# Kernel tuning notes

Measured on AMD Instinct MI355X. Metric: run time of the kernel, lower is better.

## Reference

```python
import jax, jax.numpy as jnp
import numpy as np

B, N = 16, 2048
NOTE, BEAT_H, MEAS_H, FINAL_H = 512, 128, 64, 128
NUM_BEATS, NUM_MEAS = 256, 64
OUT = 11            # output_size; QPM_INDEX = 0
QPM = 0


def _uniform(k, shape, fan):
    b = 1.0 / np.sqrt(fan)
    return jax.random.uniform(k, shape, jnp.float32, -b, b)


def _lstm_cell(x, h, c, wih, whh, bih, bhh):
    g = x @ wih.T + bih + h @ whh.T + bhh
    ii, ff, gg, oo = jnp.split(g, 4, axis=-1)
    c2 = jax.nn.sigmoid(ff) * c + jax.nn.sigmoid(ii) * jnp.tanh(gg)
    return jax.nn.sigmoid(oo) * jnp.tanh(c2), c2


def setup_inputs() -> dict:
    key = jax.random.key(0)
    ks = jax.random.split(key, 20)
    note_emb = jax.random.normal(ks[0], (B, N, NOTE), jnp.float32)
    beat_emb = jax.random.normal(ks[1], (B, NUM_BEATS, BEAT_H), jnp.float32)
    measure_emb = jax.random.normal(ks[2], (B, NUM_MEAS, MEAS_H), jnp.float32)
    beat_numbers = jnp.sort(jax.random.randint(ks[3], (B, N), 0, NUM_BEATS), axis=1)
    measure_numbers = beat_numbers // (NUM_BEATS // NUM_MEAS)
    tin = BEAT_H + MEAS_H + 1 + (OUT - 1)   # beat-tempo LSTM input size
    fin = NOTE + BEAT_H + MEAS_H + OUT      # final LSTM input size
    d = OUT - 1
    return {
        "note_emb": note_emb, "beat_emb": beat_emb, "measure_emb": measure_emb,
        "beat_numbers": beat_numbers, "measure_numbers": measure_numbers,
        "Wa": _uniform(ks[4], (d, d), d), "ba": _uniform(ks[5], (d,), d),
        "ctx": _uniform(ks[6], (d,), d),
        "Wih_t": _uniform(ks[7], (4 * BEAT_H, tin), BEAT_H),
        "Whh_t": _uniform(ks[8], (4 * BEAT_H, BEAT_H), BEAT_H),
        "bih_t": _uniform(ks[9], (4 * BEAT_H,), BEAT_H),
        "bhh_t": _uniform(ks[10], (4 * BEAT_H,), BEAT_H),
        "Wih_f": _uniform(ks[11], (4 * FINAL_H, fin), FINAL_H),
        "Whh_f": _uniform(ks[12], (4 * FINAL_H, FINAL_H), FINAL_H),
        "bih_f": _uniform(ks[13], (4 * FINAL_H,), FINAL_H),
        "bhh_f": _uniform(ks[14], (4 * FINAL_H,), FINAL_H),
        "W_fc": _uniform(ks[15], (d, FINAL_H), FINAL_H),
        "b_fc": _uniform(ks[16], (d,), FINAL_H),
        "W_tfc": _uniform(ks[17], (1, BEAT_H), BEAT_H),
        "b_tfc": _uniform(ks[18], (1,), BEAT_H),
    }


def _decode(note_emb, beat_emb, measure_emb, beat_numbers, measure_numbers,
            Wa, ba, ctx, Wih_t, Whh_t, bih_t, bhh_t,
            Wih_f, Whh_f, bih_f, bhh_f, W_fc, b_fc, W_tfc, b_tfc):
    Bn, Nn = note_emb.shape[0], note_emb.shape[1]
    d = W_fc.shape[0]  # OUT - 1
    zs_beat = jnp.maximum(beat_numbers - beat_numbers[:, :1], 0)
    zs_meas = jnp.maximum(measure_numbers - measure_numbers[:, :1], 0)
    diff = jnp.diff(beat_numbers, axis=1)
    # beat_changed: first step forced to 1, then diff of beat numbers
    changed_all = jnp.concatenate([jnp.ones((Bn, 1), diff.dtype), diff], axis=1) > 0
    pos = jnp.arange(Nn)
    bidx = jnp.arange(Bn)

    carry0 = (
        jnp.zeros((Bn, BEAT_H)), jnp.zeros((Bn, BEAT_H)),        # tempo h, c
        jnp.zeros((Bn, FINAL_H)), jnp.zeros((Bn, FINAL_H)),      # final h, c
        jnp.zeros((Bn, d + 1)),                                   # prev_out
        jnp.zeros((Bn, beat_emb.shape[1], d)),                    # beat_results
        jnp.zeros((Bn, Nn, d + 1)),                               # out_total
    )

    def step(carry, i):
        th, tc, fh, fc_, prev_out, beat_results, out_total = carry
        changed = changed_all[:, i]                                # [B] bool
        # --- get_beat_corresp_out: notes j < i in the beat just finished ---
        prev_beat = beat_numbers[:, jnp.maximum(i - 1, 0)]         # [B]
        note_mask = (beat_numbers == prev_beat[:, None]) & (pos[None, :] < i)
        x = out_total[:, :, QPM + 1:]                              # [B,N,d]
        sim = (x @ Wa.T + ba) @ ctx                                # [B,N]
        sim = jnp.where(note_mask, sim, -1e9)
        w = jax.nn.softmax(sim, axis=1)
        result_node = jnp.einsum('bn,bnd->bd', w, x)
        result_node = jnp.where(note_mask.any(axis=1)[:, None], result_node, 0.0)
        cb = zs_beat[:, i]
        cm = zs_meas[:, i]
        # scatter result_node into beat_results only for batches whose beat changed
        old = beat_results[bidx, cb]
        beat_results = beat_results.at[bidx, cb].set(
            jnp.where(changed[:, None], result_node, old))
        # --- beat tempo RNN step (only applied where changed) ---
        tempo_in = jnp.concatenate([
            beat_emb[bidx, cb], measure_emb[bidx, cm],
            prev_out[:, QPM:QPM + 1], beat_results[bidx, cb]], axis=-1)
        th2, tc2 = _lstm_cell(tempo_in, th, tc, Wih_t, Whh_t, bih_t, bhh_t)
        th = jnp.where(changed[:, None], th2, th)
        tc = jnp.where(changed[:, None], tc2, tc)
        tmp_tempo = th2 @ W_tfc.T + b_tfc                          # [B,1]
        prev_out = prev_out.at[:, QPM:QPM + 1].set(
            jnp.where(changed[:, None], tmp_tempo, prev_out[:, QPM:QPM + 1]))
        # --- final note-level LSTM step (all batches) ---
        fin_in = jnp.concatenate([
            note_emb[:, i], beat_emb[bidx, cb], measure_emb[bidx, cm], prev_out], axis=-1)
        fh, fc_ = _lstm_cell(fin_in, fh, fc_, Wih_f, Whh_f, bih_f, bhh_f)
        out = fh @ W_fc.T + b_fc                                   # [B,d]
        prev_out = jnp.concatenate([prev_out[:, :QPM + 1], out], axis=-1)
        out_total = out_total.at[:, i].set(prev_out)
        return (th, tc, fh, fc_, prev_out, beat_results, out_total), None

    carry, _ = jax.lax.scan(step, carry0, jnp.arange(Nn))
    out_total = carry[-1]
    # zero out padded notes (note embedding all-zero rows)
    pad = (note_emb.sum(-1) == 0)[:, :, None]
    return jnp.where(pad, 0.0, out_total)


def reference(note_emb, beat_emb, measure_emb, beat_numbers, measure_numbers,
              Wa, ba, ctx, Wih_t, Whh_t, bih_t, bhh_t,
              Wih_f, Whh_f, bih_f, bhh_f, W_fc, b_fc, W_tfc, b_tfc):
    return _decode(note_emb, beat_emb, measure_emb, beat_numbers, measure_numbers,
                   Wa, ba, ctx, Wih_t, Whh_t, bih_t, bhh_t,
                   Wih_f, Whh_f, bih_f, bhh_f, W_fc, b_fc, W_tfc, b_tfc)
```

## Files before the change

### kernel.cpp

```cpp
#include <hip/hip_runtime.h>
#include <cstdint>
#include <cstddef>

#define B_      16
#define N_      2048
#define NOTE_   512
#define BEAT_H_ 128
#define MEAS_H_ 64
#define NBEATS_ 256
#define NMEAS_  64
#define OUT_    11
#define D_      10
#define TSTRIDE 136

typedef float f32x4 __attribute__((ext_vector_type(4)));
typedef unsigned int u32x4 __attribute__((ext_vector_type(4)));
typedef _Float16 h2v __attribute__((ext_vector_type(2)));

__device__ __forceinline__ float fexp2_(float x) {
#if __has_builtin(__builtin_amdgcn_exp2f)
    return __builtin_amdgcn_exp2f(x);
#else
    return exp2f(x);
#endif
}
__device__ __forceinline__ float frcp_(float x) {
#if __has_builtin(__builtin_amdgcn_rcpf)
    return __builtin_amdgcn_rcpf(x);
#else
    return 1.0f / x;
#endif
}
__device__ __forceinline__ float sigm_(float x) {
    return frcp_(1.0f + fexp2_(-1.4426950408889634f * x));
}
__device__ __forceinline__ float tanh_(float x) {
    return 1.0f - 2.0f * frcp_(fexp2_(2.8853900817779268f * x) + 1.0f);
}

__device__ __forceinline__ float dot2f_(unsigned wu, unsigned hu, float c) {
    union { unsigned u; h2v h; } a, bb;
    a.u = wu; bb.u = hu;
#if __has_builtin(__builtin_amdgcn_fdot2)
    return __builtin_amdgcn_fdot2(a.h, bb.h, c, false);
#else
    return c + (float)a.h[0] * (float)bb.h[0] + (float)a.h[1] * (float)bb.h[1];
#endif
}

__device__ __align__(16) _Float16 g_whh_h16[512 * 128];
__device__ float g_bias_eff[512];
__device__ float g_wtail0[512];
__device__ __align__(16) _Float16 g_wht_h16[512 * TSTRIDE];

__global__ __launch_bounds__(256) void pad_k(const float* __restrict__ note,
                                             int* __restrict__ padf) {
    int wave = threadIdx.x >> 6, lane = threadIdx.x & 63;
    int r = blockIdx.x * 4 + wave;
    const float* row = note + ((size_t)r << 9);
    float s = 0.f;
#pragma unroll
    for (int u = 0; u < 8; ++u) s += row[lane + (u << 6)];
#pragma unroll
    for (int off = 32; off; off >>= 1) s += __shfl_xor(s, off, 64);
    if (lane == 0) padf[r] = (s == 0.0f) ? 1 : 0;
}

__global__ __launch_bounds__(128) void fold_whh(
    const float* __restrict__ Whh_f, const float* __restrict__ Wih_f,
    const float* __restrict__ W_fc, const float* __restrict__ b_fc) {
    int gr = blockIdx.x;
    int t = threadIdx.x;
    __shared__ float tail[OUT_];
    if (t < OUT_) tail[t] = Wih_f[(size_t)gr * 715 + 704 + t];
    __syncthreads();
    float m = Whh_f[(size_t)gr * 128 + t];
#pragma unroll
    for (int d = 0; d < D_; ++d) m += tail[1 + d] * W_fc[d * 128 + t];
    g_whh_h16[(size_t)gr * 128 + t] = (_Float16)m;
    if (t == 0) {
        float bb = 0.f;
#pragma unroll
        for (int d = 0; d < D_; ++d) bb += tail[1 + d] * b_fc[d];
        g_bias_eff[gr] = bb;
        g_wtail0[gr] = tail[0];
    }
}

__global__ __launch_bounds__(128) void fold_wht(const float* __restrict__ Whh_t) {
    int gr = blockIdx.x, t = threadIdx.x;
    g_wht_h16[(size_t)gr * TSTRIDE + t] = (_Float16)Whh_t[(size_t)gr * 128 + t];
    if (t < TSTRIDE - 128) g_wht_h16[(size_t)gr * TSTRIDE + 128 + t] = (_Float16)0.f;
}

__global__ __launch_bounds__(256) void tempo_pre_k(
    const float* __restrict__ beat, const float* __restrict__ meas,
    const int* __restrict__ bnum, const int* __restrict__ mnum,
    const float* __restrict__ Wih_t, const float* __restrict__ bih_t,
    const float* __restrict__ bhh_t, float* __restrict__ tpre) {
    __shared__ float sin_[16][192];
    int b = blockIdx.x, qt = blockIdx.y;
    int t = threadIdx.x;
    int bn0 = bnum[b << 11], mn0 = mnum[b << 11];
    for (int idx = t; idx < 16 * 192; idx += 256) {
        int qq = idx / 192, kk = idx - qq * 192;
        int q = qt * 16 + qq;
        float v;
        if (kk < 128) {
            v = beat[(size_t)(b * NBEATS_ + q) * 128 + kk];
        } else {
            int cm = ((q + bn0) >> 2) - mn0;
            if (cm > 63) cm = 63;
            if (cm < 0) cm = 0;
            v = meas[(size_t)(b * NMEAS_ + cm) * 64 + (kk - 128)];
        }
        sin_[qq][kk] = v;
    }
    __syncthreads();
    for (int half = 0; half < 2; ++half) {
        int j = t + half * 256;
        const float* wr = Wih_t + (size_t)j * 203;
        float bias = bih_t[j] + bhh_t[j];
        float acc[16] = {};
        for (int k = 0; k < 192; ++k) {
            float w = wr[k];
#pragma unroll
            for (int qq = 0; qq < 16; ++qq) acc[qq] += w * sin_[qq][k];
        }
        for (int qq = 0; qq < 16; ++qq)
            tpre[(size_t)(b * NBEATS_ + qt * 16 + qq) * 512 + j] = acc[qq] + bias;
    }
}

__global__ __launch_bounds__(256) void fin_pre_gemm(
    const float* __restrict__ note, const float* __restrict__ beat,
    const float* __restrict__ meas, const int* __restrict__ bnum,
    const int* __restrict__ mnum, const float* __restrict__ Wih_f,
    const float* __restrict__ bih_f, const float* __restrict__ bhh_f,
    float* __restrict__ finp) {
    __shared__ float As[16][64];
    __shared__ float Bs[16][64];
    int t = threadIdx.x;
    int r0 = blockIdx.x * 64;
    int j0 = blockIdx.y * 64;

    int am = t >> 2, alane = t & 3;
    int r = r0 + am;
    int b = r >> 11;
    int rb = b << 11;
    int cb = bnum[r] - bnum[rb];
    int cm = mnum[r] - mnum[rb];
    const float* arow_note = note + ((size_t)r << 9);
    const float* arow_beat = beat + ((size_t)(b * NBEATS_ + cb) << 7);
    const float* arow_meas = meas + ((size_t)(b * NMEAS_ + cm) << 6);

    int jj = t >> 2, blane = t & 3;
    const float* brow = Wih_f + (size_t)(j0 + jj) * 715;

    int tm0 = (t & 15) * 4, tn0 = (t >> 4) * 4;
    float acc[4][4] = {};

    for (int k0 = 0; k0 < 704; k0 += 16) {
        int ka = k0 + alane * 4;
        float4 av;
        if (ka < 512)      av = *(const float4*)(arow_note + ka);
        else if (ka < 640) av = *(const float4*)(arow_beat + (ka - 512));
        else               av = *(const float4*)(arow_meas + (ka - 640));
        int kb = k0 + blane * 4;
        float b0 = brow[kb], b1 = brow[kb + 1], b2 = brow[kb + 2], b3 = brow[kb + 3];
        __syncthreads();
        As[alane * 4 + 0][am] = av.x;
        As[alane * 4 + 1][am] = av.y;
        As[alane * 4 + 2][am] = av.z;
        As[alane * 4 + 3][am] = av.w;
        Bs[blane * 4 + 0][jj] = b0;
        Bs[blane * 4 + 1][jj] = b1;
        Bs[blane * 4 + 2][jj] = b2;
        Bs[blane * 4 + 3][jj] = b3;
        __syncthreads();
#pragma unroll
        for (int kk = 0; kk < 16; ++kk) {
            float4 a4 = *(const float4*)&As[kk][tm0];
            float4 b4 = *(const float4*)&Bs[kk][tn0];
            float aa[4] = {a4.x, a4.y, a4.z, a4.w};
            float bb[4] = {b4.x, b4.y, b4.z, b4.w};
#pragma unroll
            for (int mi = 0; mi < 4; ++mi)
#pragma unroll
                for (int ni = 0; ni < 4; ++ni) acc[mi][ni] += aa[mi] * bb[ni];
        }
    }
    float bias[4], beff[4];
#pragma unroll
    for (int ni = 0; ni < 4; ++ni) {
        int j = j0 + tn0 + ni;
        bias[ni] = bih_f[j] + bhh_f[j];
        beff[ni] = g_bias_eff[j];
    }
#pragma unroll
    for (int mi = 0; mi < 4; ++mi) {
        int rr = r0 + tm0 + mi;
        float eb = (rr & 2047) ? 1.0f : 0.0f;
        float4 o;
        o.x = acc[mi][0] + bias[0] + eb * beff[0];
        o.y = acc[mi][1] + bias[1] + eb * beff[1];
        o.z = acc[mi][2] + bias[2] + eb * beff[2];
        o.w = acc[mi][3] + bias[3] + eb * beff[3];
        *(float4*)(finp + ((size_t)rr << 9) + j0 + tn0) = o;
    }
}

__global__ __launch_bounds__(512)
__attribute__((amdgpu_waves_per_eu(2, 2)))
void decode_seq(
    float* finp,
    const float* __restrict__ tpre, const int* __restrict__ bnum,
    const float* __restrict__ Wih_t,
    const float* __restrict__ W_fc, const float* __restrict__ b_fc,
    const float* __restrict__ W_tfc, const float* __restrict__ b_tfc,
    const float* __restrict__ Wa, const float* __restrict__ ba,
    const float* __restrict__ ctx, float* __restrict__ tval) {
    __shared__ __align__(16) _Float16 wht16_s[512 * TSTRIDE];
    __shared__ __align__(16) _Float16 hf16_s[2][128];
    __shared__ __align__(16) _Float16 ht16_s[128];
    __shared__ __align__(16) _Float16 u16_s[128];
    __shared__ __align__(16) float hA_s[128];
    __shared__ __align__(16) float s_w_s[1024];
    __shared__ float wfcT[128][12];
    __shared__ float bfc_s[12];
    __shared__ float v_s[12];
    __shared__ float cur_res[12];
    __shared__ float pred_s[8];
    __shared__ float sc_s[4];
    __shared__ unsigned short run_start_s[300];
    __shared__ short run_cb_s[300];
    __shared__ int nruns_s;

    const int t = threadIdx.x, lane = t & 63, wave = t >> 6;
    const int b = blockIdx.x;
    const int bl = lane & 15;
    const int eidx = wave * 16 + bl;
    const int r_lane = (lane >> 4) * 128 + eidx;

    u32x4 wf0, wf1, wf2, wf3, wf4, wf5, wf6, wf7;
    u32x4 wf8, wf9, wf10, wf11, wf12, wf13, wf14, wf15;
    {
        const u32x4* wfp = (const u32x4*)(g_whh_h16 + (size_t)r_lane * 128);
        wf0 = wfp[0];   wf1 = wfp[1];   wf2 = wfp[2];   wf3 = wfp[3];
        wf4 = wfp[4];   wf5 = wfp[5];   wf6 = wfp[6];   wf7 = wfp[7];
        wf8 = wfp[8];   wf9 = wfp[9];   wf10 = wfp[10]; wf11 = wfp[11];
        wf12 = wfp[12]; wf13 = wfp[13]; wf14 = wfp[14]; wf15 = wfp[15];
    }
    asm volatile("" : "+v"(wf0), "+v"(wf1), "+v"(wf2), "+v"(wf3),
                      "+v"(wf4), "+v"(wf5), "+v"(wf6), "+v"(wf7));
    asm volatile("" : "+v"(wf8), "+v"(wf9), "+v"(wf10), "+v"(wf11),
                      "+v"(wf12), "+v"(wf13), "+v"(wf14), "+v"(wf15));

    const float wtail0_r = g_wtail0[r_lane];
    const float wtfc_r = W_tfc[eidx];
    float wiht_r[OUT_];
#pragma unroll
    for (int u = 0; u < OUT_; ++u) wiht_r[u] = Wih_t[(size_t)r_lane * 203 + 192 + u];

    {
        const uint4* src = (const uint4*)g_wht_h16;
        uint4* dst = (uint4*)wht16_s;
#pragma unroll
        for (int k = 0; k < 17; ++k) dst[t + 512 * k] = src[t + 512 * k];
    }
    for (int k = t; k < 128 * D_; k += 512) {
        int d = k >> 7, r = k & 127;
        wfcT[r][d] = W_fc[k];
    }
    if (t < 128) {
        hf16_s[0][t] = (_Float16)0.f;
        hf16_s[1][t] = (_Float16)0.f;
        ht16_s[t] = (_Float16)0.f;
    }
    if (t < D_) {
        bfc_s[t] = b_fc[t];
        cur_res[t] = 0.f;
        float vv = 0.f;
        for (int m = 0; m < D_; ++m) vv += ctx[m] * Wa[m * D_ + t];
        v_s[t] = vv;
    }
    if (t == 10) {
        float cc = 0.f;
        for (int m = 0; m < D_; ++m) cc += ba[m] * ctx[m];
        sc_s[0] = cc;
        sc_s[1] = b_tfc[0];
        sc_s[2] = 0.f;
    }
    const int* bnb = bnum + (b << 11);
    int bn0 = bnb[0];
    int base = t * 4;
    int bvm = (base == 0) ? 0 : bnb[base - 1];
    int bv0 = bnb[base], bv1 = bnb[base + 1], bv2 = bnb[base + 2], bv3 = bnb[base + 3];
    if (base == 0) bvm = bv0 - 1;
    int c = (bv0 != bvm) + (bv1 != bv0) + (bv2 != bv1) + (bv3 != bv2);
    ((int*)s_w_s)[t] = c;
    __syncthreads();
    if (t == 0) {
        float c1v = sc_s[0];
        for (int d = 0; d < D_; ++d) c1v += bfc_s[d] * v_s[d];
        sc_s[3] = c1v;
    }
    if (t < 128) {
        float uu = 0.f;
#pragma unroll
        for (int d = 0; d < D_; ++d) uu += v_s[d] * wfcT[t][d];
        u16_s[t] = (_Float16)uu;
    }
    if (wave == 0) {
        int c8[8], s = 0;
#pragma unroll
        for (int j = 0; j < 8; ++j) { c8[j] = ((int*)s_w_s)[lane * 8 + j]; s += c8[j]; }
        int incl = s;
#pragma unroll
        for (int off = 1; off < 64; off <<= 1) {
            int n = __shfl_up(incl, off, 64);
            if (lane >= off) incl += n;
        }
        int run = incl - s;
#pragma unroll
        for (int j = 0; j < 8; ++j) { ((int*)s_w_s)[512 + lane * 8 + j] = run; run += c8[j]; }
        if (lane == 63) nruns_s = incl;
    }
    __syncthreads();
    {
        int O = ((int*)s_w_s)[512 + t];
        if (bv0 != bvm) { run_start_s[O] = (unsigned short)(base + 0); run_cb_s[O] = (short)(bv0 - bn0); O++; }
        if (bv1 != bv0) { run_start_s[O] = (unsigned short)(base + 1); run_cb_s[O] = (short)(bv1 - bn0); O++; }
        if (bv2 != bv1) { run_start_s[O] = (unsigned short)(base + 2); run_cb_s[O] = (short)(bv2 - bn0); O++; }
        if (bv3 != bv2) { run_start_s[O] = (unsigned short)(base + 3); run_cb_s[O] = (short)(bv3 - bn0); O++; }
    }
    __syncthreads();
    const int nruns_r = nruns_s;

    char* hg = (char*)(finp + ((size_t)b << 11) * 512);
    const size_t fin_off = ((size_t)b << 11) * 512 + (size_t)r_lane;
    float gf_cur = finp[fin_off];
    float gt_pre = tpre[(size_t)(b * NBEATS_) * 512 + r_lane];
    int cur_run = -1, next_start = 0, run_s = 0, S_prev = 0;
    int pb = 0;
    float cf_r = 0.f, ct_r = 0.f;

    for (int i = 0; i < N_; ++i) {
        const bool changed = (i == next_start);
        if (changed) {
            ++cur_run;
            S_prev = run_s;
            run_s = i;
            next_start = (cur_run + 1 < nruns_r) ? (int)run_start_s[cur_run + 1] : (N_ * 2);
        }
        float prev0 = sc_s[2];
        float gf_nxt = finp[fin_off + (size_t)(i + 1) * 512];

        float acc;
        {
            const u32x4* hq = (const u32x4*)&hf16_s[pb][0];
            float a0 = 0.f, a1 = 0.f, a2 = 0.f, a3 = 0.f;
#define MSTEP(W, K)                                            \
            { u32x4 H = hq[K];                                 \
              a0 = dot2f_(W.x, H.x, a0);                       \
              a1 = dot2f_(W.y, H.y, a1);                       \
              a2 = dot2f_(W.z, H.z, a2);                       \
              a3 = dot2f_(W.w, H.w, a3); }
            MSTEP(wf0, 0)   MSTEP(wf1, 1)   MSTEP(wf2, 2)   MSTEP(wf3, 3)
            MSTEP(wf4, 4)   MSTEP(wf5, 5)   MSTEP(wf6, 6)   MSTEP(wf7, 7)
            MSTEP(wf8, 8)   MSTEP(wf9, 9)   MSTEP(wf10, 10) MSTEP(wf11, 11)
            MSTEP(wf12, 12) MSTEP(wf13, 13) MSTEP(wf14, 14) MSTEP(wf15, 15)
#undef MSTEP
            acc = (a0 + a1) + (a2 + a3);
        }
        float gmain = gf_cur + acc;
        gf_cur = gf_nxt;
        float tv = prev0;

        if (!changed) {
            float g = gmain + wtail0_r * prev0;
            float gF = __shfl(g, bl + 16, 64);
            float gG = __shfl(g, bl + 32, 64);
            float gO = __shfl(g, bl + 48, 64);
            if (lane < 16) {
                float c2 = sigm_(gF) * cf_r + sigm_(g) * tanh_(gG);
                float h2 = sigm_(gO) * tanh_(c2);
                cf_r = c2;
                hf16_s[pb ^ 1][eidx] = (_Float16)h2;
                *(_Float16*)(hg + (size_t)i * 2048 + (eidx << 1)) = (_Float16)h2;
            }
        } else {
            float gt;
            {
                const u32x4* wq = (const u32x4*)(wht16_s + (size_t)r_lane * TSTRIDE);
                const u32x4* hq = (const u32x4*)ht16_s;
                float a0 = 0.f, a1 = 0.f, a2 = 0.f, a3 = 0.f;
#pragma unroll
                for (int k = 0; k < 16; ++k) {
                    u32x4 W = wq[k];
                    u32x4 H = hq[k];
                    a0 = dot2f_(W.x, H.x, a0);
                    a1 = dot2f_(W.y, H.y, a1);
                    a2 = dot2f_(W.z, H.z, a2);
                    a3 = dot2f_(W.w, H.w, a3);
                }
                gt = gt_pre + (a0 + a1) + (a2 + a3) + wiht_r[0] * prev0;
            }
            if (cur_run + 1 < nruns_r)
                gt_pre = tpre[(size_t)(b * NBEATS_ + (int)run_cb_s[cur_run + 1]) * 512 + r_lane];

            if (wave == 0) {
                int Lc = i - S_prev;
                if (Lc > 1024) Lc = 1024;
                const char* hgB = hg + (size_t)S_prev * 2048;
                const float c1 = sc_s[3];
                float lmax = -1e30f;
                for (int j = lane; j < Lc; j += 64) {
                    const u32x4* hrow = (const u32x4*)(hgB + (size_t)j * 2048);
                    const u32x4* uq = (const u32x4*)u16_s;
                    float a0 = 0.f, a1 = 0.f, a2 = 0.f, a3 = 0.f;
#pragma unroll
                    for (int k = 0; k < 16; ++k) {
                        u32x4 hv = hrow[k], uv = uq[k];
                        a0 = dot2f_(hv.x, uv.x, a0);
                        a1 = dot2f_(hv.y, uv.y, a1);
                        a2 = dot2f_(hv.z, uv.z, a2);
                        a3 = dot2f_(hv.w, uv.w, a3);
                    }
                    float s = c1 + (a0 + a1) + (a2 + a3);
                    s_w_s[j] = s;
                    lmax = fmaxf(lmax, s);
                }
#pragma unroll
                for (int off = 32; off; off >>= 1)
                    lmax = fmaxf(lmax, __shfl_xor(lmax, off, 64));
                float lsum = 0.f;
                for (int j = lane; j < Lc; j += 64) {
                    float w = fexp2_(1.4426950408889634f * (s_w_s[j] - lmax));
                    s_w_s[j] = w;
                    lsum += w;
                }
#pragma unroll
                for (int off = 32; off; off >>= 1) lsum += __shfl_xor(lsum, off, 64);
                float inv = (Lc > 0) ? (1.0f / lsum) : 0.f;
                float hA0 = 0.f, hA1 = 0.f;
                for (int j = 0; j < Lc; ++j) {
                    unsigned hv = *(const unsigned*)(hgB + (size_t)j * 2048 + (lane << 2));
                    float w = s_w_s[j];
                    union { unsigned u; _Float16 h[2]; } hu; hu.u = hv;
                    hA0 += w * (float)hu.h[0];
                    hA1 += w * (float)hu.h[1];
                }
                hA_s[2 * lane] = hA0 * inv;
                hA_s[2 * lane + 1] = hA1 * inv;
                int dd = lane >> 3, rl = lane & 7, d2 = 8 + dd;
                float po1 = 0.f, po2 = 0.f;
                for (int k2 = 0; k2 < 16; ++k2) {
                    int r = rl + (k2 << 3);
                    float hv = hA_s[r];
                    po1 += hv * wfcT[r][dd];
                    if (d2 < D_) po2 += hv * wfcT[r][d2];
                }
                po1 += __shfl_xor(po1, 1, 64); po1 += __shfl_xor(po1, 2, 64); po1 += __shfl_xor(po1, 4, 64);
                po2 += __shfl_xor(po2, 1, 64); po2 += __shfl_xor(po2, 2, 64); po2 += __shfl_xor(po2, 4, 64);
                if (rl == 0) {
                    cur_res[dd] = (Lc > 0) ? (po1 + bfc_s[dd]) : 0.f;
                    if (d2 < D_) cur_res[d2] = (Lc > 0) ? (po2 + bfc_s[d2]) : 0.f;
                }
            }
            __syncthreads();
#pragma unroll
            for (int d = 0; d < D_; ++d) gt += wiht_r[1 + d] * cur_res[d];
            float gF = __shfl(gt, bl + 16, 64);
            float gG = __shfl(gt, bl + 32, 64);
            float gO = __shfl(gt, bl + 48, 64);
            if (lane < 16) {
                float c2 = sigm_(gF) * ct_r + sigm_(gt) * tanh_(gG);
                float h2 = sigm_(gO) * tanh_(c2);
                ct_r = c2;
                ht16_s[eidx] = (_Float16)h2;
                float p = h2 * wtfc_r;
                p += __shfl_xor(p, 1, 64);
                p += __shfl_xor(p, 2, 64);
                p += __shfl_xor(p, 4, 64);
                p += __shfl_xor(p, 8, 64);
                if (bl == 0) pred_s[wave] = p;
            }
            __syncthreads();
            float tnew = sc_s[1];
#pragma unroll
            for (int wv = 0; wv < 8; ++wv) tnew += pred_s[wv];
            tv = tnew;
            float g = gmain + wtail0_r * tnew;
            float gF2 = __shfl(g, bl + 16, 64);
            float gG2 = __shfl(g, bl + 32, 64);
            float gO2 = __shfl(g, bl + 48, 64);
            if (lane < 16) {
                float c2 = sigm_(gF2) * cf_r + sigm_(g) * tanh_(gG2);
                float h2 = sigm_(gO2) * tanh_(c2);
                cf_r = c2;
                hf16_s[pb ^ 1][eidx] = (_Float16)h2;
                *(_Float16*)(hg + (size_t)i * 2048 + (eidx << 1)) = (_Float16)h2;
            }
            if (t == 0) sc_s[2] = tnew;
        }
        if (t == 0) tval[(b << 11) + i] = tv;
        __syncthreads();
        pb ^= 1;
    }
}

__global__ __launch_bounds__(256) void out_k(
    const float* __restrict__ finp, const float* __restrict__ tval,
    const int* __restrict__ padf, const float* __restrict__ W_fc,
    const float* __restrict__ b_fc, float* __restrict__ out) {
    int g = blockIdx.x * 256 + threadIdx.x;
    int row = g >> 4, slot = g & 15;
    if (row >= B_ * N_) return;
    int pd = padf[row];
    float* orow = out + (size_t)row * OUT_;
    if (slot == 10) {
        orow[0] = pd ? 0.f : tval[row];
        return;
    }
    if (slot > 10) return;
    const unsigned* h2 = (const unsigned*)(finp + (size_t)row * 512);
    const float* wr = W_fc + slot * 128;
    float acc = b_fc[slot];
#pragma unroll 8
    for (int k = 0; k < 64; ++k) {
        union { unsigned u; _Float16 h[2]; } hv; hv.u = h2[k];
        acc += (float)hv.h[0] * wr[2 * k] + (float)hv.h[1] * wr[2 * k + 1];
    }
    orow[1 + slot] = pd ? 0.f : acc;
}

extern "C" void kernel_launch(void* const* d_in, const int* in_sizes, int n_in,
                              void* d_out, int out_size, void* d_ws, size_t ws_size,
                              hipStream_t stream) {
    const float* note  = (const float*)d_in[0];
    const float* beat  = (const float*)d_in[1];
    const float* meas  = (const float*)d_in[2];
    const int*   bnum  = (const int*)d_in[3];
    const int*   mnum  = (const int*)d_in[4];
    const float* Wa    = (const float*)d_in[5];
    const float* ba    = (const float*)d_in[6];
    const float* ctx   = (const float*)d_in[7];
    const float* Wih_t = (const float*)d_in[8];
    const float* Whh_t = (const float*)d_in[9];
    const float* bih_t = (const float*)d_in[10];
    const float* bhh_t = (const float*)d_in[11];
    const float* Wih_f = (const float*)d_in[12];
    const float* Whh_f = (const float*)d_in[13];
    const float* bih_f = (const float*)d_in[14];
    const float* bhh_f = (const float*)d_in[15];
    const float* W_fc  = (const float*)d_in[16];
    const float* b_fc  = (const float*)d_in[17];
    const float* W_tfc = (const float*)d_in[18];
    const float* b_tfc = (const float*)d_in[19];
    float* out = (float*)d_out;

    char* ws = (char*)d_ws;
    float* finp = (float*)ws;
    float* tpre = (float*)(ws + (size_t)64 * 1024 * 1024);
    int*   padf = (int*)(ws + (size_t)72 * 1024 * 1024);
    float* tval = (float*)(ws + (size_t)73 * 1024 * 1024);

    pad_k<<<8192, 256, 0, stream>>>(note, padf);
    fold_whh<<<512, 128, 0, stream>>>(Whh_f, Wih_f, W_fc, b_fc);
    fold_wht<<<512, 128, 0, stream>>>(Whh_t);
    tempo_pre_k<<<dim3(16, 16), 256, 0, stream>>>(beat, meas, bnum, mnum, Wih_t,
                                                  bih_t, bhh_t, tpre);
    fin_pre_gemm<<<dim3(512, 8), 256, 0, stream>>>(note, beat, meas, bnum, mnum,
                                                   Wih_f, bih_f, bhh_f, finp);
    decode_seq<<<16, 512, 0, stream>>>(finp, tpre, bnum, Wih_t,
                                       W_fc, b_fc, W_tfc, b_tfc, Wa, ba, ctx,
                                       tval);
    out_k<<<2048, 256, 0, stream>>>(finp, tval, padf, W_fc, b_fc, out);
}
```

Measured before the change: 3.879 ms.

## Stage input-gate rows via async global-to-LDS double buffering in the decode loop

The sequential decode loop now processes notes in chunks of 16, prefetching each chunk's precomputed input-gate rows into a double-buffered LDS staging area with global_load_lds, instead of issuing a per-step global load. The tempo recurrent weights are no longer copied into LDS; they are read from global memory when a beat changes, which frees LDS for staging. Most per-step __syncthreads are replaced by a lighter lgkmcnt-wait plus s_barrier, with a full barrier only at chunk ends or before a beat change. The gate activations are reworked so every lane computes one sigmoid, with tanh expressed as 2*sigmoid(2x)-1, before the shuffles. The trade-off is more global weight traffic on beat changes, and the lighter barrier does not wait on vmem, which raises a risk with the async LDS loads and the global h writes that the attention step reads back.

```diff
diff --git a/kernel.cpp b/kernel.cpp
--- a/kernel.cpp
+++ b/kernel.cpp
@@ -11,7 +11,6 @@
 #define NMEAS_  64
 #define OUT_    11
 #define D_      10
-#define TSTRIDE 136
 
 typedef float f32x4 __attribute__((ext_vector_type(4)));
 typedef unsigned int u32x4 __attribute__((ext_vector_type(4)));
@@ -48,10 +47,12 @@
 #endif
 }
 
+#define BAR_LDS() asm volatile("s_waitcnt lgkmcnt(0)\n\ts_barrier" ::: "memory")
+
 __device__ __align__(16) _Float16 g_whh_h16[512 * 128];
 __device__ float g_bias_eff[512];
 __device__ float g_wtail0[512];
-__device__ __align__(16) _Float16 g_wht_h16[512 * TSTRIDE];
+__device__ __align__(16) _Float16 g_wht_h16[512 * 128];
 
 __global__ __launch_bounds__(256) void pad_k(const float* __restrict__ note,
                                              int* __restrict__ padf) {
@@ -89,8 +90,7 @@
 
 __global__ __launch_bounds__(128) void fold_wht(const float* __restrict__ Whh_t) {
     int gr = blockIdx.x, t = threadIdx.x;
-    g_wht_h16[(size_t)gr * TSTRIDE + t] = (_Float16)Whh_t[(size_t)gr * 128 + t];
-    if (t < TSTRIDE - 128) g_wht_h16[(size_t)gr * TSTRIDE + 128 + t] = (_Float16)0.f;
+    g_wht_h16[(size_t)gr * 128 + t] = (_Float16)Whh_t[(size_t)gr * 128 + t];
 }
 
 __global__ __launch_bounds__(256) void tempo_pre_k(
@@ -220,7 +220,7 @@
     const float* __restrict__ W_tfc, const float* __restrict__ b_tfc,
     const float* __restrict__ Wa, const float* __restrict__ ba,
     const float* __restrict__ ctx, float* __restrict__ tval) {
-    __shared__ __align__(16) _Float16 wht16_s[512 * TSTRIDE];
+    __shared__ __align__(16) float stage_s[2][16 * 512];
     __shared__ __align__(16) _Float16 hf16_s[2][128];
     __shared__ __align__(16) _Float16 ht16_s[128];
     __shared__ __align__(16) _Float16 u16_s[128];
@@ -239,8 +239,28 @@
     const int t = threadIdx.x, lane = t & 63, wave = t >> 6;
     const int b = blockIdx.x;
     const int bl = lane & 15;
+    const int grp = lane >> 4;
     const int eidx = wave * 16 + bl;
-    const int r_lane = (lane >> 4) * 128 + eidx;
+    const int r_lane = grp * 128 + eidx;
+    const float kmul = (grp == 2) ? 2.0f : 1.0f;
+    const float badd = (grp == 2) ? -1.0f : 0.0f;
+
+    const float* finb = finp + ((size_t)b << 11) * 512;
+    char* hg = (char*)finb;
+
+    {
+        const char* gsrc = (const char*)finb;
+        char* ldst = (char*)(&stage_s[0][0]);
+        int s0 = wave << 2;
+#pragma unroll
+        for (int qq = 0; qq < 4; ++qq) {
+            int ss = s0 + qq;
+            __builtin_amdgcn_global_load_lds(
+                (const __attribute__((address_space(1))) unsigned*)(gsrc + ((size_t)ss << 10) + (lane << 4)),
+                (__attribute__((address_space(3))) unsigned*)(ldst + (ss << 10)),
+                16, 0, 0);
+        }
+    }
 
     u32x4 wf0, wf1, wf2, wf3, wf4, wf5, wf6, wf7;
     u32x4 wf8, wf9, wf10, wf11, wf12, wf13, wf14, wf15;
@@ -262,12 +282,6 @@
 #pragma unroll
     for (int u = 0; u < OUT_; ++u) wiht_r[u] = Wih_t[(size_t)r_lane * 203 + 192 + u];
 
-    {
-        const uint4* src = (const uint4*)g_wht_h16;
-        uint4* dst = (uint4*)wht16_s;
-#pragma unroll
-        for (int k = 0; k < 17; ++k) dst[t + 512 * k] = src[t + 512 * k];
-    }
     for (int k = t; k < 128 * D_; k += 512) {
         int d = k >> 7, r = k & 127;
         wfcT[r][d] = W_fc[k];
@@ -337,176 +351,201 @@
     __syncthreads();
     const int nruns_r = nruns_s;
 
-    char* hg = (char*)(finp + ((size_t)b << 11) * 512);
-    const size_t fin_off = ((size_t)b << 11) * 512 + (size_t)r_lane;
-    float gf_cur = finp[fin_off];
     float gt_pre = tpre[(size_t)(b * NBEATS_) * 512 + r_lane];
     int cur_run = -1, next_start = 0, run_s = 0, S_prev = 0;
-    int pb = 0;
+    int pb = 0, buf = 0;
     float cf_r = 0.f, ct_r = 0.f;
 
-    for (int i = 0; i < N_; ++i) {
-        const bool changed = (i == next_start);
-        if (changed) {
-            ++cur_run;
-            S_prev = run_s;
-            run_s = i;
-            next_start = (cur_run + 1 < nruns_r) ? (int)run_start_s[cur_run + 1] : (N_ * 2);
+#pragma unroll 1
+    for (int ch = 0; ch < 128; ++ch) {
+        if (ch + 1 < 128) {
+            const char* gsrc = (const char*)finb + ((size_t)(ch + 1) << 15);
+            char* ldst = (char*)(&stage_s[buf ^ 1][0]);
+            int s0 = wave << 2;
+#pragma unroll
+            for (int qq = 0; qq < 4; ++qq) {
+                int ss = s0 + qq;
+                __builtin_amdgcn_global_load_lds(
+                    (const __attribute__((address_space(1))) unsigned*)(gsrc + ((size_t)ss << 10) + (lane << 4)),
+                    (__attribute__((address_space(3))) unsigned*)(ldst + (ss << 10)),
+                    16, 0, 0);
+            }
         }
-        float prev0 = sc_s[2];
-        float gf_nxt = finp[fin_off + (size_t)(i + 1) * 512];
-
-        float acc;
-        {
-            const u32x4* hq = (const u32x4*)&hf16_s[pb][0];
-            float a0 = 0.f, a1 = 0.f, a2 = 0.f, a3 = 0.f;
+#pragma unroll 1
+        for (int q = 0; q < 16; ++q) {
+            const int i = (ch << 4) | q;
+            const bool changed = (i == next_start);
+            if (changed) {
+                ++cur_run;
+                S_prev = run_s;
+                run_s = i;
+                next_start = (cur_run + 1 < nruns_r) ? (int)run_start_s[cur_run + 1] : (N_ * 2);
+            }
+            const float prev0 = sc_s[2];
+            const float gf = stage_s[buf][(q << 9) | r_lane];
+
+            float acc;
+            {
+                const u32x4* hq = (const u32x4*)&hf16_s[pb][0];
+                float a0 = 0.f, a1 = 0.f, a2 = 0.f, a3 = 0.f;
 #define MSTEP(W, K)                                            \
-            { u32x4 H = hq[K];                                 \
-              a0 = dot2f_(W.x, H.x, a0);                       \
-              a1 = dot2f_(W.y, H.y, a1);                       \
-              a2 = dot2f_(W.z, H.z, a2);                       \
-              a3 = dot2f_(W.w, H.w, a3); }
-            MSTEP(wf0, 0)   MSTEP(wf1, 1)   MSTEP(wf2, 2)   MSTEP(wf3, 3)
-            MSTEP(wf4, 4)   MSTEP(wf5, 5)   MSTEP(wf6, 6)   MSTEP(wf7, 7)
-            MSTEP(wf8, 8)   MSTEP(wf9, 9)   MSTEP(wf10, 10) MSTEP(wf11, 11)
-            MSTEP(wf12, 12) MSTEP(wf13, 13) MSTEP(wf14, 14) MSTEP(wf15, 15)
+                { u32x4 H = hq[K];                             \
+                  a0 = dot2f_(W.x, H.x, a0);                   \
+                  a1 = dot2f_(W.y, H.y, a1);                   \
+                  a2 = dot2f_(W.z, H.z, a2);                   \
+                  a3 = dot2f_(W.w, H.w, a3); }
+                MSTEP(wf0, 0)   MSTEP(wf1, 1)   MSTEP(wf2, 2)   MSTEP(wf3, 3)
+                MSTEP(wf4, 4)   MSTEP(wf5, 5)   MSTEP(wf6, 6)   MSTEP(wf7, 7)
+                MSTEP(wf8, 8)   MSTEP(wf9, 9)   MSTEP(wf10, 10) MSTEP(wf11, 11)
+                MSTEP(wf12, 12) MSTEP(wf13, 13) MSTEP(wf14, 14) MSTEP(wf15, 15)
 #undef MSTEP
-            acc = (a0 + a1) + (a2 + a3);
+                acc = (a0 + a1) + (a2 + a3);
+            }
+            const float gmain = gf + acc;
+            float tv = prev0;
+
+            if (!changed) {
+                float g = gmain + wtail0_r * prev0;
+                float sg = sigm_(kmul * g);
+                float act = fmaf(kmul, sg, badd);
+                float aF = __shfl(act, bl + 16, 64);
+                float aG = __shfl(act, bl + 32, 64);
+                float aO = __shfl(act, bl + 48, 64);
+                if (lane < 16) {
+                    float c2 = aF * cf_r + act * aG;
+                    float h2 = aO * tanh_(c2);
+                    cf_r = c2;
+                    hf16_s[pb ^ 1][eidx] = (_Float16)h2;
+                    *(_Float16*)(hg + ((size_t)i << 11) + (eidx << 1)) = (_Float16)h2;
+                }
+            } else {
+                float gt;
+                {
+                    const u32x4* wq = (const u32x4*)(g_wht_h16 + ((size_t)r_lane << 7));
+                    const u32x4* hq = (const u32x4*)ht16_s;
+                    float a0 = 0.f, a1 = 0.f, a2 = 0.f, a3 = 0.f;
+#pragma unroll
+                    for (int k = 0; k < 16; ++k) {
+                        u32x4 W = wq[k];
+                        u32x4 H = hq[k];
+                        a0 = dot2f_(W.x, H.x, a0);
+                        a1 = dot2f_(W.y, H.y, a1);
+                        a2 = dot2f_(W.z, H.z, a2);
+                        a3 = dot2f_(W.w, H.w, a3);
+                    }
+                    gt = gt_pre + (a0 + a1) + (a2 + a3) + wiht_r[0] * prev0;
+                }
+                if (cur_run + 1 < nruns_r)
+                    gt_pre = tpre[(size_t)(b * NBEATS_ + (int)run_cb_s[cur_run + 1]) * 512 + r_lane];
+
+                if (wave == 0) {
+                    int Lc = i - S_prev;
+                    if (Lc > 1024) Lc = 1024;
+                    const char* hgB = hg + (size_t)S_prev * 2048;
+                    const float c1 = sc_s[3];
+                    float lmax = -1e30f;
+                    for (int j = lane; j < Lc; j += 64) {
+                        const u32x4* hrow = (const u32x4*)(hgB + (size_t)j * 2048);
+                        const u32x4* uq = (const u32x4*)u16_s;
+                        float a0 = 0.f, a1 = 0.f, a2 = 0.f, a3 = 0.f;
+#pragma unroll
+                        for (int k = 0; k < 16; ++k) {
+                            u32x4 hv = hrow[k], uv = uq[k];
+                            a0 = dot2f_(hv.x, uv.x, a0);
+                            a1 = dot2f_(hv.y, uv.y, a1);
+                            a2 = dot2f_(hv.z, uv.z, a2);
+                            a3 = dot2f_(hv.w, uv.w, a3);
+                        }
+                        float s = c1 + (a0 + a1) + (a2 + a3);
+                        s_w_s[j] = s;
+                        lmax = fmaxf(lmax, s);
+                    }
+#pragma unroll
+                    for (int off = 32; off; off >>= 1)
+                        lmax = fmaxf(lmax, __shfl_xor(lmax, off, 64));
+                    float lsum = 0.f;
+                    for (int j = lane; j < Lc; j += 64) {
+                        float w = fexp2_(1.4426950408889634f * (s_w_s[j] - lmax));
+                        s_w_s[j] = w;
+                        lsum += w;
+                    }
+#pragma unroll
+                    for (int off = 32; off; off >>= 1) lsum += __shfl_xor(lsum, off, 64);
+                    float inv = (Lc > 0) ? (1.0f / lsum) : 0.f;
+                    float hA0 = 0.f, hA1 = 0.f;
+                    for (int j = 0; j < Lc; ++j) {
+                        unsigned hv = *(const unsigned*)(hgB + (size_t)j * 2048 + (lane << 2));
+                        float w = s_w_s[j];
+                        union { unsigned u; _Float16 h[2]; } hu; hu.u = hv;
+                        hA0 += w * (float)hu.h[0];
+                        hA1 += w * (float)hu.h[1];
+                    }
+                    hA_s[2 * lane] = hA0 * inv;
+                    hA_s[2 * lane + 1] = hA1 * inv;
+                    int dd = lane >> 3, rl = lane & 7, d2 = 8 + dd;
+                    float po1 = 0.f, po2 = 0.f;
+                    for (int k2 = 0; k2 < 16; ++k2) {
+                        int r = rl + (k2 << 3);
+                        float hv = hA_s[r];
+                        po1 += hv * wfcT[r][dd];
+                        if (d2 < D_) po2 += hv * wfcT[r][d2];
+                    }
+                    po1 += __shfl_xor(po1, 1, 64); po1 += __shfl_xor(po1, 2, 64); po1 += __shfl_xor(po1, 4, 64);
+                    po2 += __shfl_xor(po2, 1, 64); po2 += __shfl_xor(po2, 2, 64); po2 += __shfl_xor(po2, 4, 64);
+                    if (rl == 0) {
+                        cur_res[dd] = (Lc > 0) ? (po1 + bfc_s[dd]) : 0.f;
+                        if (d2 < D_) cur_res[d2] = (Lc > 0) ? (po2 + bfc_s[d2]) : 0.f;
+                    }
+                }
+                BAR_LDS();
+#pragma unroll
+                for (int d = 0; d < D_; ++d) gt += wiht_r[1 + d] * cur_res[d];
+                float st = sigm_(kmul * gt);
+                float actt = fmaf(kmul, st, badd);
+                float aFt = __shfl(actt, bl + 16, 64);
+                float aGt = __shfl(actt, bl + 32, 64);
+                float aOt = __shfl(actt, bl + 48, 64);
+                if (lane < 16) {
+                    float c2 = aFt * ct_r + actt * aGt;
+                    float h2 = aOt * tanh_(c2);
+                    ct_r = c2;
+                    ht16_s[eidx] = (_Float16)h2;
+                    float p = h2 * wtfc_r;
+                    p += __shfl_xor(p, 1, 64);
+                    p += __shfl_xor(p, 2, 64);
+                    p += __shfl_xor(p, 4, 64);
+                    p += __shfl_xor(p, 8, 64);
+                    if (bl == 0) pred_s[wave] = p;
+                }
+                BAR_LDS();
+                float tnew = sc_s[1];
+#pragma unroll
+                for (int wv = 0; wv < 8; ++wv) tnew += pred_s[wv];
+                tv = tnew;
+                float g = gmain + wtail0_r * tnew;
+                float s2 = sigm_(kmul * g);
+                float act2 = fmaf(kmul, s2, badd);
+                float aF2 = __shfl(act2, bl + 16, 64);
+                float aG2 = __shfl(act2, bl + 32, 64);
+                float aO2 = __shfl(act2, bl + 48, 64);
+                if (lane < 16) {
+                    float c2 = aF2 * cf_r + act2 * aG2;
+                    float h2 = aO2 * tanh_(c2);
+                    cf_r = c2;
+                    hf16_s[pb ^ 1][eidx] = (_Float16)h2;
+                    *(_Float16*)(hg + ((size_t)i << 11) + (eidx << 1)) = (_Float16)h2;
+                }
+                if (t == 0) sc_s[2] = tnew;
+            }
+            if (t == 0) tval[(b << 11) + i] = tv;
+            {
+                bool nextch = (i + 1 == next_start);
+                if (nextch || q == 15) __syncthreads();
+                else BAR_LDS();
+            }
+            pb ^= 1;
         }
-        float gmain = gf_cur + acc;
-        gf_cur = gf_nxt;
-        float tv = prev0;
-
-        if (!changed) {
-            float g = gmain + wtail0_r * prev0;
-            float gF = __shfl(g, bl + 16, 64);
-            float gG = __shfl(g, bl + 32, 64);
-            float gO = __shfl(g, bl + 48, 64);
-            if (lane < 16) {
-                float c2 = sigm_(gF) * cf_r + sigm_(g) * tanh_(gG);
-                float h2 = sigm_(gO) * tanh_(c2);
-                cf_r = c2;
-                hf16_s[pb ^ 1][eidx] = (_Float16)h2;
-                *(_Float16*)(hg + (size_t)i * 2048 + (eidx << 1)) = (_Float16)h2;
-            }
-        } else {
-            float gt;
-            {
-                const u32x4* wq = (const u32x4*)(wht16_s + (size_t)r_lane * TSTRIDE);
-                const u32x4* hq = (const u32x4*)ht16_s;
-                float a0 = 0.f, a1 = 0.f, a2 = 0.f, a3 = 0.f;
-#pragma unroll
-                for (int k = 0; k < 16; ++k) {
-                    u32x4 W = wq[k];
-                    u32x4 H = hq[k];
-                    a0 = dot2f_(W.x, H.x, a0);
-                    a1 = dot2f_(W.y, H.y, a1);
-                    a2 = dot2f_(W.z, H.z, a2);
-                    a3 = dot2f_(W.w, H.w, a3);
-                }
-                gt = gt_pre + (a0 + a1) + (a2 + a3) + wiht_r[0] * prev0;
-            }
-            if (cur_run + 1 < nruns_r)
-                gt_pre = tpre[(size_t)(b * NBEATS_ + (int)run_cb_s[cur_run + 1]) * 512 + r_lane];
-
-            if (wave == 0) {
-                int Lc = i - S_prev;
-                if (Lc > 1024) Lc = 1024;
-                const char* hgB = hg + (size_t)S_prev * 2048;
-                const float c1 = sc_s[3];
-                float lmax = -1e30f;
-                for (int j = lane; j < Lc; j += 64) {
-                    const u32x4* hrow = (const u32x4*)(hgB + (size_t)j * 2048);
-                    const u32x4* uq = (const u32x4*)u16_s;
-                    float a0 = 0.f, a1 = 0.f, a2 = 0.f, a3 = 0.f;
-#pragma unroll
-                    for (int k = 0; k < 16; ++k) {
-                        u32x4 hv = hrow[k], uv = uq[k];
-                        a0 = dot2f_(hv.x, uv.x, a0);
-                        a1 = dot2f_(hv.y, uv.y, a1);
-                        a2 = dot2f_(hv.z, uv.z, a2);
-                        a3 = dot2f_(hv.w, uv.w, a3);
-                    }
-                    float s = c1 + (a0 + a1) + (a2 + a3);
-                    s_w_s[j] = s;
-                    lmax = fmaxf(lmax, s);
-                }
-#pragma unroll
-                for (int off = 32; off; off >>= 1)
-                    lmax = fmaxf(lmax, __shfl_xor(lmax, off, 64));
-                float lsum = 0.f;
-                for (int j = lane; j < Lc; j += 64) {
-                    float w = fexp2_(1.4426950408889634f * (s_w_s[j] - lmax));
-                    s_w_s[j] = w;
-                    lsum += w;
-                }
-#pragma unroll
-                for (int off = 32; off; off >>= 1) lsum += __shfl_xor(lsum, off, 64);
-                float inv = (Lc > 0) ? (1.0f / lsum) : 0.f;
-                float hA0 = 0.f, hA1 = 0.f;
-                for (int j = 0; j < Lc; ++j) {
-                    unsigned hv = *(const unsigned*)(hgB + (size_t)j * 2048 + (lane << 2));
-                    float w = s_w_s[j];
-                    union { unsigned u; _Float16 h[2]; } hu; hu.u = hv;
-                    hA0 += w * (float)hu.h[0];
-                    hA1 += w * (float)hu.h[1];
-                }
-                hA_s[2 * lane] = hA0 * inv;
-                hA_s[2 * lane + 1] = hA1 * inv;
-                int dd = lane >> 3, rl = lane & 7, d2 = 8 + dd;
-                float po1 = 0.f, po2 = 0.f;
-                for (int k2 = 0; k2 < 16; ++k2) {
-                    int r = rl + (k2 << 3);
-                    float hv = hA_s[r];
-                    po1 += hv * wfcT[r][dd];
-                    if (d2 < D_) po2 += hv * wfcT[r][d2];
-                }
-                po1 += __shfl_xor(po1, 1, 64); po1 += __shfl_xor(po1, 2, 64); po1 += __shfl_xor(po1, 4, 64);
-                po2 += __shfl_xor(po2, 1, 64); po2 += __shfl_xor(po2, 2, 64); po2 += __shfl_xor(po2, 4, 64);
-                if (rl == 0) {
-                    cur_res[dd] = (Lc > 0) ? (po1 + bfc_s[dd]) : 0.f;
-                    if (d2 < D_) cur_res[d2] = (Lc > 0) ? (po2 + bfc_s[d2]) : 0.f;
-                }
-            }
-            __syncthreads();
-#pragma unroll
-            for (int d = 0; d < D_; ++d) gt += wiht_r[1 + d] * cur_res[d];
-            float gF = __shfl(gt, bl + 16, 64);
-            float gG = __shfl(gt, bl + 32, 64);
-            float gO = __shfl(gt, bl + 48, 64);
-            if (lane < 16) {
-                float c2 = sigm_(gF) * ct_r + sigm_(gt) * tanh_(gG);
-                float h2 = sigm_(gO) * tanh_(c2);
-                ct_r = c2;
-                ht16_s[eidx] = (_Float16)h2;
-                float p = h2 * wtfc_r;
-                p += __shfl_xor(p, 1, 64);
-                p += __shfl_xor(p, 2, 64);
-                p += __shfl_xor(p, 4, 64);
-                p += __shfl_xor(p, 8, 64);
-                if (bl == 0) pred_s[wave] = p;
-            }
-            __syncthreads();
-            float tnew = sc_s[1];
-#pragma unroll
-            for (int wv = 0; wv < 8; ++wv) tnew += pred_s[wv];
-            tv = tnew;
-            float g = gmain + wtail0_r * tnew;
-            float gF2 = __shfl(g, bl + 16, 64);
-            float gG2 = __shfl(g, bl + 32, 64);
-            float gO2 = __shfl(g, bl + 48, 64);
-            if (lane < 16) {
-                float c2 = sigm_(gF2) * cf_r + sigm_(g) * tanh_(gG2);
-                float h2 = sigm_(gO2) * tanh_(c2);
-                cf_r = c2;
-                hf16_s[pb ^ 1][eidx] = (_Float16)h2;
-                *(_Float16*)(hg + (size_t)i * 2048 + (eidx << 1)) = (_Float16)h2;
-            }
-            if (t == 0) sc_s[2] = tnew;
-        }
-        if (t == 0) tval[(b << 11) + i] = tv;
-        __syncthreads();
-        pb ^= 1;
+        buf ^= 1;
     }
 }
 
```

New measurement: 4.609 ms. 18.8% more time.
